# Optimization experiments

Hardware: AMD Instinct MI355X
Metric: run time of the kernel (lower is better)

## Reference

```python
import jax, jax.numpy as jnp
import numpy as np

D_MODEL = 1024
N_HEADS = 16
HEAD_DIM = D_MODEL // N_HEADS


def setup_inputs() -> dict:
    key = jax.random.key(0)
    ks = jax.random.split(key, 5)
    T, B = 2048, 2
    scale = 1.0 / np.sqrt(D_MODEL)
    x = jax.random.normal(ks[0], (T, B, D_MODEL), dtype=jnp.float32)
    W_qkv = jax.random.normal(ks[1], (D_MODEL, 3 * D_MODEL), dtype=jnp.float32) * scale
    b_qkv = jnp.zeros((3 * D_MODEL,), dtype=jnp.float32)
    W_out = jax.random.normal(ks[2], (D_MODEL, D_MODEL), dtype=jnp.float32) * scale
    b_out = jnp.zeros((D_MODEL,), dtype=jnp.float32)
    return {"x": x, "W_qkv": W_qkv, "b_qkv": b_qkv, "W_out": W_out, "b_out": b_out}


def reference(x, W_qkv, b_qkv, W_out, b_out):
    T, B, D = x.shape
    H, Dh = N_HEADS, HEAD_DIM
    qkv = x @ W_qkv + b_qkv  # [T, B, 3D]
    q, k, v = jnp.split(qkv, 3, axis=-1)
    # [T, B, D] -> [B, H, T, Dh]
    def to_heads(t):
        return t.reshape(T, B, H, Dh).transpose(1, 2, 0, 3)
    q, k, v = to_heads(q), to_heads(k), to_heads(v)
    scores = jnp.einsum("bhqd,bhkd->bhqk", q, k) / jnp.sqrt(jnp.float32(Dh))
    causal = jnp.tril(jnp.ones((T, T), dtype=bool))  # True where attention allowed
    scores = jnp.where(causal, scores, -jnp.inf)
    attn = jax.nn.softmax(scores, axis=-1)
    context = jnp.einsum("bhqk,bhkd->bhqd", attn, v)  # [B, H, T, Dh]
    context = context.transpose(2, 0, 1, 3).reshape(T, B, D)  # [T, B, D]
    return context @ W_out + b_out
```

## Files before the change

### kernel.cpp

```cpp
#include <hip/hip_runtime.h>
#include <stdint.h>

#define T_SEQ 2048
#define BATCH 2
#define DMODEL 1024
#define NH 16
#define DH 64
#define M_ROWS (T_SEQ * BATCH)
#define N_QKV (3 * DMODEL)
#define BHQ (32 * T_SEQ)

typedef unsigned short u16;
using bf16x8 = __attribute__((ext_vector_type(8))) __bf16;
using f32x4  = __attribute__((ext_vector_type(4))) float;

__device__ __forceinline__ u16 f2bf(float f) {
    union { float f; uint32_t u; } v; v.f = f;
    uint32_t r = v.u + 0x7fffu + ((v.u >> 16) & 1u);
    return (u16)(r >> 16);
}

__device__ __forceinline__ uint32_t pack2(float a, float b) {
    union { float f; uint32_t u; } x, y; x.f = a; y.f = b;
    return (x.u >> 16) | (y.u & 0xffff0000u);
}

__device__ __forceinline__ float bf2f(u16 u) {
    union { uint32_t u; float f; } v; v.u = (uint32_t)u << 16;
    return v.f;
}

__device__ __forceinline__ void lds_load16(void* lds, const void* g) {
    auto lp = (__attribute__((address_space(3))) uint32_t*)(uint32_t)(uintptr_t)lds;
    auto gp = (const __attribute__((address_space(1))) uint32_t*)(uintptr_t)g;
    __builtin_amdgcn_global_load_lds(gp, lp, 16, 0, 0);
}

#define SCQ 0.18033688011112f


__global__ void cvt4_kernel(const float* __restrict__ in, u16* __restrict__ out, int n4) {
    int i = blockIdx.x * 256 + threadIdx.x;
    if (i < n4) {
        float4 v = ((const float4*)in)[i];
        union { u16 u[4]; uint2 d; } o;
        o.u[0] = f2bf(v.x); o.u[1] = f2bf(v.y); o.u[2] = f2bf(v.z); o.u[3] = f2bf(v.w);
        ((uint2*)out)[i] = o.d;
    }
}

__global__ void cvt_t2_kernel(const float* __restrict__ A, u16* __restrict__ oA,
                              const float* __restrict__ B, u16* __restrict__ oB) {
    __shared__ float t[32][33];
    const int R = 1024;
    const float* in; u16* out; int C, bx;
    if (blockIdx.x < 96) { in = A; out = oA; C = 3072; bx = blockIdx.x * 32; }
    else                 { in = B; out = oB; C = 1024; bx = (blockIdx.x - 96) * 32; }
    int by = blockIdx.y * 32;
    int tx = threadIdx.x & 31, ty = threadIdx.x >> 5;
#pragma unroll
    for (int rr = 0; rr < 32; rr += 8)
        t[ty + rr][tx] = in[(size_t)(by + ty + rr) * C + bx + tx];
    __syncthreads();
#pragma unroll
    for (int rr = 0; rr < 32; rr += 8)
        out[(size_t)(bx + ty + rr) * R + by + tx] = f2bf(t[tx][ty + rr]);
}


template<int EPI, int NF>
__global__ __launch_bounds__(256) void gemm_kernel(
    const u16* __restrict__ A, const u16* __restrict__ Bt,
    const float* __restrict__ bias,
    u16* __restrict__ outQ, u16* __restrict__ outK, u16* __restrict__ outV,
    float* __restrict__ outF,
    int M, int N, int K)
{
    __shared__ __align__(16) u16 lA[2][128 * 32];
    __shared__ __align__(16) u16 lB[2][NF * 32 * 32];

    const int tid  = threadIdx.x;
    const int bm   = blockIdx.y * 128;
    const int bn   = blockIdx.x * (NF * 32);
    const int lane = tid & 63;
    const int wid  = tid >> 6;
    const int wm   = (wid >> 1) * 64;
    const int wn   = (wid & 1) * (NF * 16);
    const int qr   = lane & 15;
    const int quad = lane >> 4;
    const int r4   = lane >> 2;
    const int c4   = (((lane & 3) ^ ((r4 >> 1) & 3))) * 8;
    const int sw   = (qr >> 1) & 3;

    f32x4 acc[4][NF];
#pragma unroll
    for (int i = 0; i < 4; i++)
#pragma unroll
        for (int j = 0; j < NF; j++) acc[i][j] = f32x4{0.f, 0.f, 0.f, 0.f};

#pragma unroll
    for (int cc = 0; cc < 2; cc++) {
        int c = wid + cc * 4;
        lds_load16(&lA[0][c * 512], &A[(size_t)(bm + 16 * c + r4) * K + c4]);
    }
#pragma unroll
    for (int c = wid; c < 2 * NF; c += 4)
        lds_load16(&lB[0][c * 512], &Bt[(size_t)(bn + 16 * c + r4) * K + c4]);

    int p = 0;
    for (int k0 = 0; k0 < K; k0 += 32, p ^= 1) {
        __syncthreads();
        if (k0 + 32 < K) {
            int nb = p ^ 1;
#pragma unroll
            for (int cc = 0; cc < 2; cc++) {
                int c = wid + cc * 4;
                lds_load16(&lA[nb][c * 512], &A[(size_t)(bm + 16 * c + r4) * K + k0 + 32 + c4]);
            }
#pragma unroll
            for (int c = wid; c < 2 * NF; c += 4)
                lds_load16(&lB[nb][c * 512], &Bt[(size_t)(bn + 16 * c + r4) * K + k0 + 32 + c4]);
        }

        bf16x8 af[4], bfr[NF];
#pragma unroll
        for (int i = 0; i < 4; i++)
            af[i] = *(const bf16x8*)&lA[p][(wm + i * 16 + qr) * 32 + ((quad ^ sw) * 8)];
#pragma unroll
        for (int j = 0; j < NF; j++)
            bfr[j] = *(const bf16x8*)&lB[p][(wn + j * 16 + qr) * 32 + ((quad ^ sw) * 8)];
#pragma unroll
        for (int i = 0; i < 4; i++)
#pragma unroll
            for (int j = 0; j < NF; j++)
                acc[i][j] = __builtin_amdgcn_mfma_f32_16x16x32_bf16(af[i], bfr[j], acc[i][j], 0, 0, 0);
    }

#pragma unroll
    for (int i = 0; i < 4; i++) {
#pragma unroll
        for (int j = 0; j < NF; j++) {
            int col = bn + wn + j * 16 + qr;
            float bv = bias[col];
#pragma unroll
            for (int r = 0; r < 4; r++) {
                int row = bm + wm + i * 16 + quad * 4 + r;
                float val = acc[i][j][r] + bv;
                if (EPI == 0) {
                    int t = row >> 1, b = row & 1;
                    int which = col >> 10;
                    int dm = col & 1023;
                    int h = dm >> 6, dh = dm & 63;
                    int bh = b * NH + h;
                    if (which == 0) {
                        outQ[((size_t)bh * T_SEQ + t) * DH + dh] = f2bf(val * SCQ);
                    } else if (which == 1) {
                        outK[((size_t)bh * T_SEQ + t) * DH + dh] = f2bf(val);
                    } else {
                        outV[((size_t)bh * DH + dh) * T_SEQ + t] = f2bf(val);
                    }
                } else {
                    outF[(size_t)row * N + col] = val;
                }
            }
        }
    }
}


__global__ __launch_bounds__(256) void attn_kernel(
    const u16* __restrict__ Qb, const u16* __restrict__ Kb,
    const u16* __restrict__ Vt,
    u16* __restrict__ Op, float* __restrict__ Lp)
{
    __shared__ __align__(16) u16 lK[2][64 * 64];
    __shared__ __align__(16) u16 lV[2][64 * 64];
    __shared__ __align__(16) u16 lP[4][16 * 64];

    const int bh   = blockIdx.x;
    const int y    = blockIdx.y;
    const int qt   = (y < 8) ? 15 - y : y - 8;
    const int seg  = blockIdx.z;
    const int tid  = threadIdx.x;
    const int lane = tid & 63;
    const int wid  = tid >> 6;
    const int qr   = lane & 15;
    const int quad = lane >> 4;
    const int sw   = qr & 7;

    const int srow = wid * 8 + (lane >> 3);
    const int scol = (((lane & 7) ^ ((lane >> 3) & 7))) * 8;

    const u16* Q  = Qb + (size_t)bh * T_SEQ * DH;
    const u16* Kp = Kb + (size_t)bh * T_SEQ * DH;
    const u16* Vp = Vt + (size_t)bh * DH * T_SEQ;

    const int q0 = qt * 128 + wid * 32;

    bf16x8 qf[2][2];
#pragma unroll
    for (int g = 0; g < 2; g++)
#pragma unroll
        for (int ks = 0; ks < 2; ks++)
            qf[g][ks] = *(const bf16x8*)&Q[(size_t)(q0 + g * 16 + qr) * DH + ks * 32 + quad * 8];

    bf16x8 onesf;
#pragma unroll
    for (int j = 0; j < 8; j++) onesf[j] = (__bf16)1.0f;

    f32x4 o[2][5];
#pragma unroll
    for (int g = 0; g < 2; g++)
#pragma unroll
        for (int f = 0; f < 5; f++) o[g][f] = f32x4{0.f, 0.f, 0.f, 0.f};

    const int kt0 = seg * (qt + 1);
    const int kt1 = kt0 + (qt + 1);

#pragma unroll
    for (int half = 0; half < 2; half++) {
        lds_load16(&lK[0][half * 2048 + wid * 512],
                   &Kp[(size_t)(kt0 * 64 + half * 32 + srow) * DH + scol]);
        lds_load16(&lV[0][half * 2048 + wid * 512],
                   &Vp[(size_t)(half * 32 + srow) * T_SEQ + kt0 * 64 + scol]);
    }

    int p = 0;
    for (int kt = kt0; kt < kt1; kt++, p ^= 1) {
        __syncthreads();
        if (kt + 1 < kt1) {
            int nb = p ^ 1;
#pragma unroll
            for (int half = 0; half < 2; half++) {
                lds_load16(&lK[nb][half * 2048 + wid * 512],
                           &Kp[(size_t)((kt + 1) * 64 + half * 32 + srow) * DH + scol]);
                lds_load16(&lV[nb][half * 2048 + wid * 512],
                           &Vp[(size_t)(half * 32 + srow) * T_SEQ + (kt + 1) * 64 + scol]);
            }
        }
        if (kt * 64 > q0 + 31) continue;

        f32x4 s[2][4];
#pragma unroll
        for (int g = 0; g < 2; g++)
#pragma unroll
            for (int fn = 0; fn < 4; fn++) s[g][fn] = f32x4{0.f, 0.f, 0.f, 0.f};
#pragma unroll
        for (int fn = 0; fn < 4; fn++)
#pragma unroll
            for (int ks = 0; ks < 2; ks++) {
                bf16x8 kf = *(const bf16x8*)&lK[p][(fn * 16 + qr) * 64 + (((ks * 4 + quad) ^ sw) * 8)];
#pragma unroll
                for (int g = 0; g < 2; g++)
                    s[g][fn] = __builtin_amdgcn_mfma_f32_16x16x32_bf16(kf, qf[g][ks], s[g][fn], 0, 0, 0);
            }

        if (kt * 64 + 63 > q0) {
#pragma unroll
            for (int g = 0; g < 2; g++) {
                int q = q0 + g * 16 + qr;
#pragma unroll
                for (int fn = 0; fn < 4; fn++) {
                    int key = kt * 64 + fn * 16 + quad * 4;
#pragma unroll
                    for (int r = 0; r < 4; r++)
                        if (key + r > q) s[g][fn][r] = -1e30f;
                }
            }
        }

        bf16x8 pf[2][2];
#pragma unroll
        for (int g = 0; g < 2; g++) {
#pragma unroll
            for (int fn = 0; fn < 4; fn++) {
                float p0 = exp2f(s[g][fn][0]);
                float p1 = exp2f(s[g][fn][1]);
                float p2 = exp2f(s[g][fn][2]);
                float p3 = exp2f(s[g][fn][3]);
                uint2 w; w.x = pack2(p0, p1); w.y = pack2(p2, p3);
                int phys = ((fn * 2 + (quad >> 1)) ^ sw);
                *(uint2*)&lP[wid][qr * 64 + phys * 8 + (quad & 1) * 4] = w;
            }
#pragma unroll
            for (int ks = 0; ks < 2; ks++)
                pf[g][ks] = *(const bf16x8*)&lP[wid][qr * 64 + (((ks * 4 + quad) ^ sw) * 8)];
        }

#pragma unroll
        for (int f = 0; f < 5; f++)
#pragma unroll
            for (int ks = 0; ks < 2; ks++) {
                bf16x8 vf = (f == 4) ? onesf
                    : *(const bf16x8*)&lV[p][(f * 16 + qr) * 64 + (((ks * 4 + quad) ^ sw) * 8)];
#pragma unroll
                for (int g = 0; g < 2; g++)
                    o[g][f] = __builtin_amdgcn_mfma_f32_16x16x32_bf16(vf, pf[g][ks], o[g][f], 0, 0, 0);
            }
    }

#pragma unroll
    for (int g = 0; g < 2; g++) {
        int q = q0 + g * 16 + qr;
        size_t rbase = (size_t)seg * BHQ + (size_t)bh * T_SEQ + q;
        if (quad == 0) Lp[rbase] = o[g][4][0];
#pragma unroll
        for (int f = 0; f < 4; f++) {
            uint2 w;
            w.x = (uint32_t)f2bf(o[g][f][0]) | ((uint32_t)f2bf(o[g][f][1]) << 16);
            w.y = (uint32_t)f2bf(o[g][f][2]) | ((uint32_t)f2bf(o[g][f][3]) << 16);
            *(uint2*)&Op[rbase * 64 + f * 16 + quad * 4] = w;
        }
    }
}


__global__ void merge_kernel(const u16* __restrict__ Op, const float* __restrict__ Lp,
                             u16* __restrict__ ctx)
{
    int idx = blockIdx.x * 256 + threadIdx.x;
    int fq  = idx & 15;
    int q   = (idx >> 4) & (T_SEQ - 1);
    int bh  = idx >> 15;
    int b = bh >> 4, h = bh & 15;
    size_t rbase = (size_t)bh * T_SEQ + q;

    float invl = 1.0f / (Lp[rbase] + Lp[rbase + BHQ]);
    union { uint2 d; u16 u[4]; } a, c, r;
    a.d = *(const uint2*)&Op[rbase * 64 + fq * 4];
    c.d = *(const uint2*)&Op[(rbase + BHQ) * 64 + fq * 4];
#pragma unroll
    for (int i = 0; i < 4; i++)
        r.u[i] = f2bf((bf2f(a.u[i]) + bf2f(c.u[i])) * invl);
    *(uint2*)&ctx[((size_t)q * BATCH + b) * DMODEL + h * DH + fq * 4] = r.d;
}


extern "C" void kernel_launch(void* const* d_in, const int* in_sizes, int n_in,
                              void* d_out, int out_size, void* d_ws, size_t ws_size,
                              hipStream_t stream) {
    const float* x     = (const float*)d_in[0];
    const float* W_qkv = (const float*)d_in[1];
    const float* b_qkv = (const float*)d_in[2];
    const float* W_out = (const float*)d_in[3];
    const float* b_out = (const float*)d_in[4];
    float* out = (float*)d_out;

    char* ws = (char*)d_ws;
    u16* xb     = (u16*)(ws + 0);
    u16* wqkv_t = (u16*)(ws + (8u  << 20));
    u16* wout_t = (u16*)(ws + (14u << 20));
    u16* Qb     = (u16*)(ws + (16u << 20));
    u16* Kb     = (u16*)(ws + (24u << 20));
    u16* Vt     = (u16*)(ws + (32u << 20));
    float* Lp   = (float*)(ws + (40u << 20));
    u16* ctx    = xb;
    u16* Op     = (u16*)d_out;

    cvt4_kernel  <<<(M_ROWS * DMODEL / 4) / 256, 256, 0, stream>>>(x, xb, M_ROWS * DMODEL / 4);
    cvt_t2_kernel<<<dim3(128, 32), 256, 0, stream>>>(W_qkv, wqkv_t, W_out, wout_t);

    gemm_kernel<0, 4><<<dim3(N_QKV / 128, M_ROWS / 128), 256, 0, stream>>>(
        xb, wqkv_t, b_qkv, Qb, Kb, Vt, nullptr, M_ROWS, N_QKV, DMODEL);

    attn_kernel<<<dim3(BATCH * NH, T_SEQ / 128, 2), 256, 0, stream>>>(
        Qb, Kb, Vt, Op, Lp);

    merge_kernel<<<(BHQ * 16) / 256, 256, 0, stream>>>(Op, Lp, ctx);

    gemm_kernel<1, 2><<<dim3(DMODEL / 64, M_ROWS / 128), 256, 0, stream>>>(
        ctx, wout_t, b_out, nullptr, nullptr, nullptr, out, M_ROWS, DMODEL, DMODEL);
}
```

Baseline: 187.3 us.

## Add 256x256-tile 8-wave QKV GEMM with swizzled LDS and interleaved staging

Replaces the generic 128x128 QKV projection GEMM with a dedicated kernel that uses 256x256 output tiles, 512 threads (8 waves, 2x4 layout), K-step 64, XOR-swizzled LDS layout and a block-index swizzle for L2 locality. Global-to-LDS loads for the next K-step are interleaved between four MFMA phases with explicit barriers, waitcnts and wave priority hints. The goal is more data reuse per LDS byte and better overlap of memory with MFMA. The cost is heavy register pressure (128 accumulators per thread), only 192 blocks to fill the CUs, and fragile hand-placed synchronisation.

```diff
diff --git a/kernel.cpp b/kernel.cpp
--- a/kernel.cpp
+++ b/kernel.cpp
@@ -37,6 +37,10 @@
 }
 
 #define SCQ 0.18033688011112f
+
+#define SBAR()       asm volatile("s_barrier" ::: "memory")
+#define WAIT_LGKM0() asm volatile("s_waitcnt lgkmcnt(0)" ::: "memory")
+#define WAIT_VM(n)   asm volatile("s_waitcnt vmcnt(" #n ")" ::: "memory")
 
 
 __global__ void cvt4_kernel(const float* __restrict__ in, u16* __restrict__ out, int n4) {
@@ -65,6 +69,164 @@
 #pragma unroll
     for (int rr = 0; rr < 32; rr += 8)
         out[(size_t)(bx + ty + rr) * R + by + tx] = f2bf(t[tx][ty + rr]);
+}
+
+
+__global__ __launch_bounds__(512, 2) void gemm_qkv_kernel(
+    const u16* __restrict__ A, const u16* __restrict__ Bt,
+    const float* __restrict__ bias,
+    u16* __restrict__ outQ, u16* __restrict__ outK, u16* __restrict__ outV)
+{
+    __shared__ __align__(16) u16 lA[2][16384];
+    __shared__ __align__(16) u16 lB[2][16384];
+
+    const int tid  = threadIdx.x;
+    const int lane = tid & 63;
+    const int wid  = tid >> 6;
+    const int wm   = wid >> 2;
+    const int wn   = wid & 3;
+    const int qr   = lane & 15;
+    const int quad = lane >> 4;
+
+    const int swz = (blockIdx.x & 7) * 24 + (blockIdx.x >> 3);
+    const int bm  = (swz & 15) * 256;
+    const int bn  = (swz >> 4) * 256;
+
+    const int lch  = (tid & 7) ^ ((tid >> 3) & 7);
+    const int goff = (tid >> 3) * 1024 + lch * 8;
+
+    const u16* A0g = A   + (size_t)bm * 1024;
+    const u16* A1g = A0g + 128 * 1024;
+    const u16* B0g = Bt  + (size_t)bn * 1024;
+    const u16* B1g = B0g + 128 * 1024;
+
+    auto stage = [&](u16* region, const u16* g) {
+        lds_load16(region + wid * 512,        g + goff);
+        lds_load16(region + 4096 + wid * 512, g + 65536 + goff);
+    };
+
+    const int sw8 = qr & 7;
+    const int pc0 = (quad ^ sw8) * 8;
+    const int pc1 = ((quad ^ sw8) ^ 4) * 8;
+    const int aBase = wm * 8192;
+    const int bBase = (wn >> 1) * 8192 + (wn & 1) * 4096;
+
+    f32x4 acc[8][4];
+#pragma unroll
+    for (int m = 0; m < 8; m++)
+#pragma unroll
+        for (int n = 0; n < 4; n++) acc[m][n] = f32x4{0.f, 0.f, 0.f, 0.f};
+
+    const int KT = DMODEL / 64;
+
+    stage(&lA[0][0],    A0g);
+    stage(&lA[0][8192], A1g);
+    stage(&lB[0][0],    B0g);
+    stage(&lB[0][8192], B1g);
+    stage(&lA[1][0],    A0g + 64);
+    stage(&lA[1][8192], A1g + 64);
+    WAIT_VM(4);
+    SBAR();
+
+    bf16x8 af[4][2], bq0[2][2], bq1[2][2];
+
+#define MFMA_Q(MB, BF, NB)                                                      \
+    __builtin_amdgcn_s_setprio(1);                                              \
+    _Pragma("unroll")                                                           \
+    for (int kk = 0; kk < 2; kk++)                                              \
+        _Pragma("unroll")                                                       \
+        for (int i = 0; i < 4; i++)                                             \
+            _Pragma("unroll")                                                   \
+            for (int j = 0; j < 2; j++)                                         \
+                acc[MB + i][NB + j] = __builtin_amdgcn_mfma_f32_16x16x32_bf16(  \
+                    af[i][kk], BF[j][kk], acc[MB + i][NB + j], 0, 0, 0);        \
+    __builtin_amdgcn_s_setprio(0);
+
+    int p = 0;
+#pragma unroll 1
+    for (int u = 0; u < KT; u++, p ^= 1) {
+        const int np = p ^ 1;
+        const u16* lAp = lA[p];
+        const u16* lBp = lB[p];
+
+#pragma unroll
+        for (int i = 0; i < 4; i++) {
+            const u16* r = lAp + aBase + (i * 16 + qr) * 64;
+            af[i][0] = *(const bf16x8*)(r + pc0);
+            af[i][1] = *(const bf16x8*)(r + pc1);
+        }
+#pragma unroll
+        for (int j = 0; j < 2; j++) {
+            const u16* r = lBp + bBase + (j * 16 + qr) * 64;
+            bq0[j][0] = *(const bf16x8*)(r + pc0);
+            bq0[j][1] = *(const bf16x8*)(r + pc1);
+        }
+        if (u + 1 < KT) stage(&lB[np][0], B0g + (u + 1) * 64);
+        SBAR();
+        WAIT_LGKM0();
+        MFMA_Q(0, bq0, 0)
+        SBAR();
+
+#pragma unroll
+        for (int j = 0; j < 2; j++) {
+            const u16* r = lBp + bBase + ((j + 2) * 16 + qr) * 64;
+            bq1[j][0] = *(const bf16x8*)(r + pc0);
+            bq1[j][1] = *(const bf16x8*)(r + pc1);
+        }
+        if (u + 1 < KT) stage(&lB[np][8192], B1g + (u + 1) * 64);
+        SBAR();
+        WAIT_LGKM0();
+        MFMA_Q(0, bq1, 2)
+        SBAR();
+
+#pragma unroll
+        for (int i = 0; i < 4; i++) {
+            const u16* r = lAp + aBase + 4096 + (i * 16 + qr) * 64;
+            af[i][0] = *(const bf16x8*)(r + pc0);
+            af[i][1] = *(const bf16x8*)(r + pc1);
+        }
+        SBAR();
+        WAIT_LGKM0();
+        MFMA_Q(4, bq0, 0)
+        SBAR();
+
+        if (u + 2 < KT) {
+            stage(&lA[p][0],    A0g + (u + 2) * 64);
+            stage(&lA[p][8192], A1g + (u + 2) * 64);
+        }
+        SBAR();
+        WAIT_LGKM0();
+        MFMA_Q(4, bq1, 2)
+        if (u + 2 < KT) { WAIT_VM(4); } else { WAIT_VM(0); }
+        SBAR();
+    }
+#undef MFMA_Q
+
+#pragma unroll
+    for (int m = 0; m < 8; m++) {
+#pragma unroll
+        for (int n = 0; n < 4; n++) {
+            int col = bn + wn * 64 + n * 16 + qr;
+            float bv = bias[col];
+            int which = col >> 10;
+            int dm = col & 1023;
+            int h = dm >> 6, dh = dm & 63;
+#pragma unroll
+            for (int r = 0; r < 4; r++) {
+                int row = bm + wm * 128 + m * 16 + quad * 4 + r;
+                float val = acc[m][n][r] + bv;
+                int t = row >> 1, b = row & 1;
+                int bh = b * NH + h;
+                if (which == 0) {
+                    outQ[((size_t)bh * T_SEQ + t) * DH + dh] = f2bf(val * SCQ);
+                } else if (which == 1) {
+                    outK[((size_t)bh * T_SEQ + t) * DH + dh] = f2bf(val);
+                } else {
+                    outV[((size_t)bh * DH + dh) * T_SEQ + t] = f2bf(val);
+                }
+            }
+        }
+    }
 }
 
 
@@ -360,8 +522,7 @@
     cvt4_kernel  <<<(M_ROWS * DMODEL / 4) / 256, 256, 0, stream>>>(x, xb, M_ROWS * DMODEL / 4);
     cvt_t2_kernel<<<dim3(128, 32), 256, 0, stream>>>(W_qkv, wqkv_t, W_out, wout_t);
 
-    gemm_kernel<0, 4><<<dim3(N_QKV / 128, M_ROWS / 128), 256, 0, stream>>>(
-        xb, wqkv_t, b_qkv, Qb, Kb, Vt, nullptr, M_ROWS, N_QKV, DMODEL);
+    gemm_qkv_kernel<<<192, 512, 0, stream>>>(xb, wqkv_t, b_qkv, Qb, Kb, Vt);
 
     attn_kernel<<<dim3(BATCH * NH, T_SEQ / 128, 2), 256, 0, stream>>>(
         Qb, Kb, Vt, Op, Lp);
```

Result: slower. 207.9 us (+11.0%).
